# Optimization experiments

Hardware: AMD Instinct MI355X
Metric: run time of the kernel (lower is better)

## Reference

```python
import jax, jax.numpy as jnp
import numpy as np

B = 2048        # batch
D_DENSE = 13    # dense input features
F = 7           # number of sparse features
CARD = 10000    # cardinality per sparse feature (== len(tokenizer_values))
E = 64          # embedding dim per feature
D_OUT = 32      # dense arch output size
S_OUT = 32      # sparse arch output size per feature
D_HID = 2 * D_OUT   # DenseArch MLP hidden (output_size*2 per code)
S_HID = 2 * S_OUT   # SparseArch MLP hidden (output_size*2 per code)
CONCAT = D_OUT + F * S_OUT    # 256
P_IN = CONCAT * CONCAT        # 65536, flattened outer product
P_HID = 512


def setup_inputs() -> dict:
    key = jax.random.key(0)
    ks = jax.random.split(key, 18)
    s = 0.05
    return {
        "dense_features": jax.random.normal(ks[0], (B, D_DENSE), dtype=jnp.float32),
        "sparse_features": jax.random.randint(ks[1], (B, F), 0, CARD, dtype=jnp.int64),
        # tokenizer_values per feature (shared arange, as in metadata)
        "tokenizers": jnp.arange(CARD, dtype=jnp.int64),
        # embedding tables stacked over features: [F, CARD, E]
        "emb_tables": jax.random.normal(ks[2], (F, CARD, E), dtype=jnp.float32) * s,
        # DenseArch MLP
        "dw1": jax.random.normal(ks[3], (D_DENSE, D_HID), dtype=jnp.float32) * s,
        "db1": jnp.zeros((D_HID,), dtype=jnp.float32),
        "dw2": jax.random.normal(ks[4], (D_HID, D_OUT), dtype=jnp.float32) * s,
        "db2": jnp.zeros((D_OUT,), dtype=jnp.float32),
        # per-feature sparse MLPs stacked over features
        "sw1": jax.random.normal(ks[5], (F, E, S_HID), dtype=jnp.float32) * s,
        "sb1": jnp.zeros((F, S_HID), dtype=jnp.float32),
        "sw2": jax.random.normal(ks[6], (F, S_HID, S_OUT), dtype=jnp.float32) * s,
        "sb2": jnp.zeros((F, S_OUT), dtype=jnp.float32),
        # PredictionLayer MLP
        "pw1": jax.random.normal(ks[7], (P_IN, P_HID), dtype=jnp.float32) * s,
        "pb1": jnp.zeros((P_HID,), dtype=jnp.float32),
        "pw2": jax.random.normal(ks[8], (P_HID, 1), dtype=jnp.float32) * s,
        "pb2": jnp.zeros((1,), dtype=jnp.float32),
    }


def reference(dense_features, sparse_features, tokenizers, emb_tables,
              dw1, db1, dw2, db2, sw1, sb1, sw2, sb2, pw1, pb1, pw2, pb2):
    # DenseArch: MLP(13 -> 64 -> 32)
    dense_out = jnp.maximum(dense_features @ dw1 + db1, 0.0) @ dw2 + db2  # [B, D_OUT]

    # SparseArch: equality-match argmax indexing (faithful to get_indices),
    # then embedding gather and per-feature MLP, vectorized over features.
    matches = sparse_features[:, :, None] == tokenizers[None, None, :]  # [B, F, CARD]
    idx = jnp.argmax(matches, axis=2)                                   # [B, F]
    gathered = emb_tables[jnp.arange(emb_tables.shape[0])[None, :], idx]  # [B, F, E]
    h = jnp.maximum(jnp.einsum('bfe,feh->bfh', gathered, sw1) + sb1, 0.0)
    sparse_out = jnp.einsum('bfh,fho->bfo', h, sw2) + sb2                # [B, F, S_OUT]

    # DenseSparseInteractionLayer: concat -> outer product -> flatten
    concat = jnp.concatenate(
        [dense_out, sparse_out.reshape(sparse_out.shape[0], -1)], axis=1)  # [B, CONCAT]
    outer = jnp.einsum('bi,bj->bij', concat, concat)
    flattened = outer.reshape(concat.shape[0], -1)                       # [B, CONCAT^2]

    # PredictionLayer: MLP(CONCAT^2 -> P_HID -> 1) + sigmoid, squeeze
    logits = jnp.maximum(flattened @ pw1 + pb1, 0.0) @ pw2 + pb2
    return jax.nn.sigmoid(logits).squeeze()
```

## Files before the change

kernel.cpp:

```cpp
#include <hip/hip_runtime.h>
#include <hip/hip_fp16.h>
#include <math.h>

#define BATCH 2048
#define NFEAT 7
#define CARD 10000
#define CONCAT 256
#define P_HID 512

#define BM 128
#define BN 128
#define BK 64
#define KSPLIT 10
#define NUNITS 640
#define UNIT_ST (512 * 64)
#define PREP_BLOCKS (NUNITS * 2)

using f16x4   = __attribute__((ext_vector_type(4))) _Float16;
using half8   = __attribute__((ext_vector_type(8))) _Float16;
using floatx4 = __attribute__((ext_vector_type(4))) float;

__device__ __forceinline__ void dma16(const _Float16* g, _Float16* l) {
    __builtin_amdgcn_global_load_lds(
        (const __attribute__((address_space(1))) unsigned int*)g,
        (__attribute__((address_space(3))) unsigned int*)l,
        16, 0, 0);
}

__device__ __forceinline__ void unit_decode(int u, int& i, int& jw) {
    if (u < 64)       { i = u;                          jw = 0; }
    else if (u < 192) { i = (u < 128) ? u : u - 128;    jw = 1; }
    else if (u < 384) { i = (u < 256) ? u - 64 : u - 256; jw = 2; }
    else              { i = (u < 448) ? u - 192 : u - 448; jw = 3; }
}

__global__ __launch_bounds__(256) void fused_pre(
    const float* __restrict__ dense, const int* __restrict__ sparse,
    const float* __restrict__ emb,
    const float* __restrict__ dw1, const float* __restrict__ db1,
    const float* __restrict__ dw2, const float* __restrict__ db2,
    const float* __restrict__ sw1, const float* __restrict__ sb1,
    const float* __restrict__ sw2, const float* __restrict__ sb2,
    const float* __restrict__ pw1,
    _Float16* __restrict__ cbf, _Float16* __restrict__ St)
{
    __shared__ __align__(16) _Float16 sh[64 * 256];
    const int tid = threadIdx.x;

    if (blockIdx.x < PREP_BLOCKS) {
        const int u = blockIdx.x >> 1, nh = blockIdx.x & 1;
        const int nb = nh * 256;
        int i, jw;
        unit_decode(u, i, jw);

#pragma unroll
        for (int m = 0; m < 16; ++m) {
            const int flat = m * 256 + tid;
            const int q = flat >> 6, c4 = flat & 63;
            const int j = (jw << 6) + q;
            floatx4 s = {0.f, 0.f, 0.f, 0.f};
            if (j >= i) {
                s = __builtin_nontemporal_load(
                    (const floatx4*)(pw1 + ((size_t)i * 256 + j) * P_HID + nb + 4 * c4));
                if (j > i) {
                    const floatx4 mv = __builtin_nontemporal_load(
                        (const floatx4*)(pw1 + ((size_t)j * 256 + i) * P_HID + nb + 4 * c4));
                    s += mv;
                }
            }
            f16x4 hv = {(_Float16)s.x, (_Float16)s.y, (_Float16)s.z, (_Float16)s.w};
            *(f16x4*)(sh + q * 256 + 4 * c4) = hv;
        }
        __syncthreads();

        const _Float16* col = sh + tid;
        _Float16* outp = St + (size_t)u * UNIT_ST + (size_t)(nb + tid) * 64;
#pragma unroll
        for (int e = 0; e < 8; ++e) {
            half8 o;
#pragma unroll
            for (int r = 0; r < 8; ++r) o[r] = col[(8 * e + r) * 256];
            *(half8*)(outp + 8 * e) = o;
        }
    } else {
        float* smem = (float*)sh;
        const int wv = tid >> 6, t = tid & 63;
        const int b = (blockIdx.x - PREP_BLOCKS) * 4 + wv;
        float* xs   = smem + wv * 13;
        float* bufA = smem + 64  + wv * 64;
        float* bufB = smem + 320 + wv * 64;

        if (t < 13) xs[t] = dense[b * 13 + t];
        __syncthreads();

        float h = db1[t];
#pragma unroll
        for (int d = 0; d < 13; ++d) h += xs[d] * dw1[d * 64 + t];
        bufA[t] = fmaxf(h, 0.f);
        __syncthreads();

        if (t < 32) {
            float o = db2[t];
#pragma unroll
            for (int k = 0; k < 64; ++k) o += bufA[k] * dw2[k * 32 + t];
            cbf[b * 256 + t] = (_Float16)o;
        }

        for (int f = 0; f < NFEAT; ++f) {
            __syncthreads();
            const int idx = sparse[b * NFEAT + f];
            bufB[t] = emb[((size_t)(f * CARD + idx)) * 64 + t];
            __syncthreads();
            float s = sb1[f * 64 + t];
#pragma unroll
            for (int e = 0; e < 64; ++e) s += bufB[e] * sw1[(f * 64 + e) * 64 + t];
            bufA[t] = fmaxf(s, 0.f);
            __syncthreads();
            if (t < 32) {
                float o = sb2[f * 32 + t];
#pragma unroll
                for (int k = 0; k < 64; ++k) o += bufA[k] * sw2[(f * 64 + k) * 32 + t];
                cbf[b * 256 + 32 + f * 32 + t] = (_Float16)o;
            }
        }
    }
}

__global__ __launch_bounds__(256, 3) void bilinear_gemm(
    const _Float16* __restrict__ cbf, const _Float16* __restrict__ St,
    _Float16* __restrict__ hidpart)
{
    __shared__ _Float16 Bl[3][BN][BK];

    const int b = blockIdx.x;
    const int xcd = b & 7, slot = b >> 3;
    const int mt = slot & 15;
    const int slice = ((slot >> 4) << 3) | xcd;
    const int nt = slice & 3, ks = slice >> 2;
    const int m0 = mt * BM, n0 = nt * BN;
    const int t0 = ks * 64;
    const int jws = (int)((0x3333222110ULL >> (ks * 4)) & 0xF);

    const int tid = threadIdx.x, lane = tid & 63, wv = tid >> 6;
    const int wrow = (wv & 1) * 64, wcol = (wv >> 1) * 64;
    const int l15 = lane & 15, l4 = lane >> 4, l7 = lane & 7;

    floatx4 acc[4][4];
#pragma unroll
    for (int i = 0; i < 4; ++i)
#pragma unroll
        for (int j = 0; j < 4; ++j) acc[i][j] = (floatx4){0.f, 0.f, 0.f, 0.f};

    const _Float16* arow0 = cbf + (size_t)(m0 + wrow + l15) * 256;

    half8 pre[4][2];
#pragma unroll
    for (int i = 0; i < 4; ++i)
#pragma unroll
        for (int kh = 0; kh < 2; ++kh)
            pre[i][kh] = *(const half8*)(arow0 + i * 4096 + (jws << 6)
                                         + kh * 32 + l4 * 8);

    const int drow = wv * 32 + (lane >> 3);
    const int eswz = (lane & 7) ^ ((lane >> 3) & 7);
    const _Float16* bsrc = St + (size_t)t0 * UNIT_ST + (size_t)(n0 + drow) * 64 + eswz * 8;

    _Float16 ciA[4], ciB[4];

    {
        int iu0, jj0; unit_decode(t0, iu0, jj0);
#pragma unroll
        for (int i = 0; i < 4; ++i) ciA[i] = arow0[i * 4096 + iu0];
    }
#pragma unroll
    for (int p = 0; p < 4; ++p)
        dma16(bsrc + (size_t)(p * 8) * 64, &Bl[0][wv * 32 + p * 8][0]);
#pragma unroll
    for (int p = 0; p < 4; ++p)
        dma16(bsrc + UNIT_ST + (size_t)(p * 8) * 64, &Bl[1][wv * 32 + p * 8][0]);
    bsrc += (size_t)2 * UNIT_ST;
    asm volatile("s_waitcnt vmcnt(4)" ::: "memory");
    __builtin_amdgcn_s_barrier();

#define GBODY(IT, CIC, CIN, CUR)                                               \
    {                                                                          \
        const int it_ = (IT);                                                  \
        const int bnx2_ = (CUR) ? (CUR) - 1 : 2;                \
        if (it_ + 1 < 64) {                                                    \
            int iu_, jj_; unit_decode(t0 + it_ + 1, iu_, jj_);                 \
            _Pragma("unroll")                                                  \
            for (int i = 0; i < 4; ++i) CIN[i] = arow0[i * 4096 + iu_];        \
        }                                                                      \
        if (it_ + 2 < 64) {                                                    \
            _Pragma("unroll")                                                  \
            for (int p = 0; p < 4; ++p)                                        \
                dma16(bsrc + (size_t)(p * 8) * 64,                             \
                      &Bl[bnx2_][wv * 32 + p * 8][0]);                         \
            bsrc += UNIT_ST;                                                   \
        }                                                                      \
        __builtin_amdgcn_s_setprio(1);                                         \
        _Pragma("unroll")                                                      \
        for (int kh = 0; kh < 2; ++kh) {                                       \
            half8 af[4], bfr[4];                                               \
            _Pragma("unroll")                                                  \
            for (int i = 0; i < 4; ++i) {                                      \
                const _Float16 c_ = CIC[i];                                    \
                const half8 cv_ = {c_, c_, c_, c_, c_, c_, c_, c_};            \
                af[i] = pre[i][kh] * cv_;                                      \
            }                                                                  \
            const int s_ = ((kh * 4 + l4) ^ l7) * 8;                           \
            _Pragma("unroll")                                                  \
            for (int j = 0; j < 4; ++j)                                        \
                bfr[j] = *(const half8*)&Bl[CUR][wcol + j * 16 + l15][s_];     \
            _Pragma("unroll")                                                  \
            for (int i = 0; i < 4; ++i)                                        \
                _Pragma("unroll")                                              \
                for (int j = 0; j < 4; ++j)                                    \
                    acc[i][j] = __builtin_amdgcn_mfma_f32_16x16x32_f16(        \
                        af[i], bfr[j], acc[i][j], 0, 0, 0);                    \
        }                                                                      \
        __builtin_amdgcn_s_setprio(0);                                         \
        if (it_ + 2 < 64)                                                      \
            asm volatile("s_waitcnt vmcnt(8)" ::: "memory");                   \
        else if (it_ + 1 < 64)                                                 \
            asm volatile("s_waitcnt vmcnt(4)" ::: "memory");                   \
        else                                                                   \
            asm volatile("s_waitcnt vmcnt(0)" ::: "memory");                   \
        __builtin_amdgcn_s_barrier();                                          \
        __builtin_amdgcn_sched_barrier(0);                                     \
    }

    int bc = 0;
    for (int it2 = 0; it2 < 64; it2 += 2) {
        GBODY(it2, ciA, ciB, bc);
        const int bc1 = (bc < 2) ? bc + 1 : 0;
        GBODY(it2 + 1, ciB, ciA, bc1);
        bc = (bc1 < 2) ? bc1 + 1 : 0;
    }
#undef GBODY

    _Float16* outp = hidpart + (size_t)ks * BATCH * P_HID;
    const int r0 = m0 + wrow + l4 * 4;
    const int c0 = n0 + wcol + l15;
#pragma unroll
    for (int i = 0; i < 4; ++i)
#pragma unroll
        for (int j = 0; j < 4; ++j)
#pragma unroll
            for (int r = 0; r < 4; ++r)
                outp[(size_t)(r0 + i * 16 + r) * P_HID + c0 + j * 16] =
                    (_Float16)acc[i][j][r];
}

__global__ __launch_bounds__(256) void finalize(
    const _Float16* __restrict__ hidpart,
    const float* __restrict__ pb1,
    const float* __restrict__ pw2,
    const float* __restrict__ pb2,
    float* __restrict__ out)
{
    const int b = blockIdx.x, t = threadIdx.x;
    const int wv = t >> 6, lane = t & 63;

    float acc[8];
#pragma unroll
    for (int k = 0; k < 8; ++k) acc[k] = 0.f;

    for (int s = wv; s < KSPLIT; s += 4) {
        const half8 v = *(const half8*)(hidpart + (size_t)s * BATCH * P_HID
                                        + (size_t)b * P_HID + lane * 8);
#pragma unroll
        for (int k = 0; k < 8; ++k) acc[k] += (float)v[k];
    }

    __shared__ float red[4 * 512];
#pragma unroll
    for (int k = 0; k < 8; ++k) red[wv * 512 + k * 64 + lane] = acc[k];
    __syncthreads();

    if (wv == 0) {
        float dot = 0.f;
#pragma unroll
        for (int k = 0; k < 8; ++k) {
            const int n = lane * 8 + k;
            float v = red[k * 64 + lane] + red[512 + k * 64 + lane]
                    + red[1024 + k * 64 + lane] + red[1536 + k * 64 + lane];
            v += pb1[n];
            v = fmaxf(v, 0.f);
            dot += v * pw2[n];
        }
#pragma unroll
        for (int off = 32; off; off >>= 1) dot += __shfl_down(dot, off, 64);
        if (lane == 0) {
            const float s = dot + pb2[0];
            out[b] = 1.f / (1.f + expf(-s));
        }
    }
}

extern "C" void kernel_launch(void* const* d_in, const int* in_sizes, int n_in,
                              void* d_out, int out_size, void* d_ws, size_t ws_size,
                              hipStream_t stream)
{
    const float* dense  = (const float*)d_in[0];
    const int*   sparse = (const int*)d_in[1];
    const float* emb = (const float*)d_in[3];
    const float* dw1 = (const float*)d_in[4];
    const float* db1 = (const float*)d_in[5];
    const float* dw2 = (const float*)d_in[6];
    const float* db2 = (const float*)d_in[7];
    const float* sw1 = (const float*)d_in[8];
    const float* sb1 = (const float*)d_in[9];
    const float* sw2 = (const float*)d_in[10];
    const float* sb2 = (const float*)d_in[11];
    const float* pw1 = (const float*)d_in[12];
    const float* pb1 = (const float*)d_in[13];
    const float* pw2 = (const float*)d_in[14];
    const float* pb2 = (const float*)d_in[15];

    char* ws = (char*)d_ws;
    _Float16* cbf     = (_Float16*)ws;
    _Float16* St      = (_Float16*)(ws + (1 << 20));
    _Float16* hidpart = (_Float16*)(ws + (1 << 20) + ((size_t)40 << 20));

    fused_pre<<<PREP_BLOCKS + BATCH / 4, 256, 0, stream>>>(
        dense, sparse, emb, dw1, db1, dw2, db2, sw1, sb1, sw2, sb2, pw1,
        cbf, St);
    bilinear_gemm<<<16 * 4 * KSPLIT, 256, 0, stream>>>(cbf, St, hidpart);
    finalize<<<BATCH, 256, 0, stream>>>(hidpart, pb1, pw2, pb2, (float*)d_out);
}
```

Before: 378.9 us.

## Enlarge bilinear GEMM tiles to 256x256 and stage scaled A in shared memory

The bilinear GEMM moves from 128x128 tiles with 4 waves to 256x256 tiles with 8 waves and 16 K-splits of 40 units each, using a new unit ordering. The scaled A operand (concat row times a per-unit scalar) is now built cooperatively into a double-buffered, swizzled LDS tile instead of being recomputed per wave in registers. B prefetch drops from triple to double buffering. The aim is more data reuse per tile and fewer redundant A multiplies, at the cost of more registers per thread, more LDS, fewer blocks in flight, and more partial sums for finalize to reduce.

```diff
diff --git a/kernel.cpp b/kernel.cpp
--- a/kernel.cpp
+++ b/kernel.cpp
@@ -8,10 +8,11 @@
 #define CONCAT 256
 #define P_HID 512
 
-#define BM 128
-#define BN 128
+#define BM 256
+#define BN 256
 #define BK 64
-#define KSPLIT 10
+#define KSPLIT 16
+#define NTILES 40
 #define NUNITS 640
 #define UNIT_ST (512 * 64)
 #define PREP_BLOCKS (NUNITS * 2)
@@ -28,10 +29,10 @@
 }
 
 __device__ __forceinline__ void unit_decode(int u, int& i, int& jw) {
-    if (u < 64)       { i = u;                          jw = 0; }
-    else if (u < 192) { i = (u < 128) ? u : u - 128;    jw = 1; }
-    else if (u < 384) { i = (u < 256) ? u - 64 : u - 256; jw = 2; }
-    else              { i = (u < 448) ? u - 192 : u - 448; jw = 3; }
+    if (u < 256)      { i = u;                jw = u >> 6; }
+    else if (u < 448) { int v = u - 256; i = v / 3;        jw = 1 + v % 3; }
+    else if (u < 576) { int v = u - 448; i = 64 + (v >> 1); jw = 2 + (v & 1); }
+    else              { i = 128 + (u - 576); jw = 3; }
 }
 
 __global__ __launch_bounds__(256) void fused_pre(
@@ -126,124 +127,142 @@
     }
 }
 
-__global__ __launch_bounds__(256, 3) void bilinear_gemm(
+__global__ __launch_bounds__(512, 2) void bilinear_gemm(
     const _Float16* __restrict__ cbf, const _Float16* __restrict__ St,
     _Float16* __restrict__ hidpart)
 {
-    __shared__ _Float16 Bl[3][BN][BK];
+    __shared__ __align__(16) _Float16 Albuf[2][BM * BK];
+    __shared__ _Float16 Bl[2][BN][BK];
 
     const int b = blockIdx.x;
     const int xcd = b & 7, slot = b >> 3;
-    const int mt = slot & 15;
-    const int slice = ((slot >> 4) << 3) | xcd;
-    const int nt = slice & 3, ks = slice >> 2;
+    const int mt = slot & 7;
+    const int slice = ((slot >> 3) << 3) | xcd;
+    const int nt = slice & 1, ks = slice >> 1;
     const int m0 = mt * BM, n0 = nt * BN;
-    const int t0 = ks * 64;
-    const int jws = (int)((0x3333222110ULL >> (ks * 4)) & 0xF);
+    const int t0 = ks * NTILES;
 
     const int tid = threadIdx.x, lane = tid & 63, wv = tid >> 6;
-    const int wrow = (wv & 1) * 64, wcol = (wv >> 1) * 64;
+    const int wrow = (wv & 1) * 128, wcol = (wv >> 1) * 64;
     const int l15 = lane & 15, l4 = lane >> 4, l7 = lane & 7;
-
-    floatx4 acc[4][4];
-#pragma unroll
-    for (int i = 0; i < 4; ++i)
+    const int arow = tid >> 1, ajoff = (tid & 1) * 32;
+
+    floatx4 acc[8][4];
+#pragma unroll
+    for (int i = 0; i < 8; ++i)
 #pragma unroll
         for (int j = 0; j < 4; ++j) acc[i][j] = (floatx4){0.f, 0.f, 0.f, 0.f};
 
-    const _Float16* arow0 = cbf + (size_t)(m0 + wrow + l15) * 256;
-
-    half8 pre[4][2];
-#pragma unroll
-    for (int i = 0; i < 4; ++i)
-#pragma unroll
-        for (int kh = 0; kh < 2; ++kh)
-            pre[i][kh] = *(const half8*)(arow0 + i * 4096 + (jws << 6)
-                                         + kh * 32 + l4 * 8);
+    const _Float16* crow = cbf + (m0 + arow) * 256;
+
+    half8 pre[4][4];
+#pragma unroll
+    for (int jw = 0; jw < 4; ++jw)
+#pragma unroll
+        for (int x = 0; x < 4; ++x)
+            pre[jw][x] = *(const half8*)(crow + (jw << 6) + ajoff + 8 * x);
+
+    const int awsz = (arow & 7) << 4;
 
     const int drow = wv * 32 + (lane >> 3);
     const int eswz = (lane & 7) ^ ((lane >> 3) & 7);
     const _Float16* bsrc = St + (size_t)t0 * UNIT_ST + (size_t)(n0 + drow) * 64 + eswz * 8;
 
-    _Float16 ciA[4], ciB[4];
+#define AGEN(NB, JW, C)                                                        \
+    {                                                                          \
+        const half8 civ_ = {C, C, C, C, C, C, C, C};                           \
+        char* aw_ = (char*)Albuf[NB] + arow * 128;                             \
+        *(half8*)(aw_ + ((ajoff * 2 +  0) ^ awsz)) = pre[JW][0] * civ_;        \
+        *(half8*)(aw_ + ((ajoff * 2 + 16) ^ awsz)) = pre[JW][1] * civ_;        \
+        *(half8*)(aw_ + ((ajoff * 2 + 32) ^ awsz)) = pre[JW][2] * civ_;        \
+        *(half8*)(aw_ + ((ajoff * 2 + 48) ^ awsz)) = pre[JW][3] * civ_;        \
+    }
+#define AGEN_SW(NB, JW, C)                                                     \
+    switch (JW) {                                                              \
+        case 0:  AGEN(NB, 0, C); break;                                        \
+        case 1:  AGEN(NB, 1, C); break;                                        \
+        case 2:  AGEN(NB, 2, C); break;                                        \
+        default: AGEN(NB, 3, C); break;                                        \
+    }
+
+    _Float16 ciA, ciB;
 
     {
-        int iu0, jj0; unit_decode(t0, iu0, jj0);
-#pragma unroll
-        for (int i = 0; i < 4; ++i) ciA[i] = arow0[i * 4096 + iu0];
-    }
-#pragma unroll
-    for (int p = 0; p < 4; ++p)
-        dma16(bsrc + (size_t)(p * 8) * 64, &Bl[0][wv * 32 + p * 8][0]);
-#pragma unroll
-    for (int p = 0; p < 4; ++p)
-        dma16(bsrc + UNIT_ST + (size_t)(p * 8) * 64, &Bl[1][wv * 32 + p * 8][0]);
-    bsrc += (size_t)2 * UNIT_ST;
-    asm volatile("s_waitcnt vmcnt(4)" ::: "memory");
+        int ui0, ujw0; unit_decode(t0, ui0, ujw0);
+        const _Float16 ci0 = crow[ui0];
+#pragma unroll
+        for (int p = 0; p < 4; ++p)
+            dma16(bsrc + (size_t)(p * 8) * 64, &Bl[0][wv * 32 + p * 8][0]);
+        bsrc += UNIT_ST;
+        AGEN_SW(0, ujw0, ci0);
+        int ui1, ujw1; unit_decode(t0 + 1, ui1, ujw1);
+        ciA = crow[ui1];
+    }
+    asm volatile("s_waitcnt vmcnt(1) lgkmcnt(0)" ::: "memory");
     __builtin_amdgcn_s_barrier();
+    __builtin_amdgcn_sched_barrier(0);
 
 #define GBODY(IT, CIC, CIN, CUR)                                               \
     {                                                                          \
         const int it_ = (IT);                                                  \
-        const int bnx2_ = (CUR) ? (CUR) - 1 : 2;                \
-        if (it_ + 1 < 64) {                                                    \
-            int iu_, jj_; unit_decode(t0 + it_ + 1, iu_, jj_);                 \
-            _Pragma("unroll")                                                  \
-            for (int i = 0; i < 4; ++i) CIN[i] = arow0[i * 4096 + iu_];        \
-        }                                                                      \
-        if (it_ + 2 < 64) {                                                    \
+        if (it_ + 1 < NTILES) {                                                \
             _Pragma("unroll")                                                  \
             for (int p = 0; p < 4; ++p)                                        \
                 dma16(bsrc + (size_t)(p * 8) * 64,                             \
-                      &Bl[bnx2_][wv * 32 + p * 8][0]);                         \
+                      &Bl[(CUR) ^ 1][wv * 32 + p * 8][0]);                     \
             bsrc += UNIT_ST;                                                   \
+            int ujw1_, ui1_; unit_decode(t0 + it_ + 1, ui1_, ujw1_);           \
+            AGEN_SW((CUR) ^ 1, ujw1_, CIC);                                    \
+        }                                                                      \
+        if (it_ + 2 < NTILES) {                                                \
+            int ui2_, ujw2_; unit_decode(t0 + it_ + 2, ui2_, ujw2_);           \
+            CIN = crow[ui2_];                                                  \
         }                                                                      \
         __builtin_amdgcn_s_setprio(1);                                         \
         _Pragma("unroll")                                                      \
         for (int kh = 0; kh < 2; ++kh) {                                       \
-            half8 af[4], bfr[4];                                               \
+            half8 af[8], bfr[4];                                               \
             _Pragma("unroll")                                                  \
-            for (int i = 0; i < 4; ++i) {                                      \
-                const _Float16 c_ = CIC[i];                                    \
-                const half8 cv_ = {c_, c_, c_, c_, c_, c_, c_, c_};            \
-                af[i] = pre[i][kh] * cv_;                                      \
+            for (int i = 0; i < 8; ++i) {                                      \
+                const int r_ = wrow + i * 16 + l15;                            \
+                const int cb_ = (kh * 64 + l4 * 16) ^ ((r_ & 7) << 4);         \
+                af[i] = *(const half8*)((const char*)Albuf[CUR] + r_ * 128 + cb_); \
             }                                                                  \
             const int s_ = ((kh * 4 + l4) ^ l7) * 8;                           \
             _Pragma("unroll")                                                  \
             for (int j = 0; j < 4; ++j)                                        \
                 bfr[j] = *(const half8*)&Bl[CUR][wcol + j * 16 + l15][s_];     \
             _Pragma("unroll")                                                  \
-            for (int i = 0; i < 4; ++i)                                        \
+            for (int i = 0; i < 8; ++i)                                        \
                 _Pragma("unroll")                                              \
                 for (int j = 0; j < 4; ++j)                                    \
                     acc[i][j] = __builtin_amdgcn_mfma_f32_16x16x32_f16(        \
                         af[i], bfr[j], acc[i][j], 0, 0, 0);                    \
         }                                                                      \
         __builtin_amdgcn_s_setprio(0);                                         \
-        if (it_ + 2 < 64)                                                      \
-            asm volatile("s_waitcnt vmcnt(8)" ::: "memory");                   \
-        else if (it_ + 1 < 64)                                                 \
-            asm volatile("s_waitcnt vmcnt(4)" ::: "memory");                   \
-        else                                                                   \
-            asm volatile("s_waitcnt vmcnt(0)" ::: "memory");                   \
-        __builtin_amdgcn_s_barrier();                                          \
-        __builtin_amdgcn_sched_barrier(0);                                     \
-    }
-
-    int bc = 0;
-    for (int it2 = 0; it2 < 64; it2 += 2) {
-        GBODY(it2, ciA, ciB, bc);
-        const int bc1 = (bc < 2) ? bc + 1 : 0;
-        GBODY(it2 + 1, ciB, ciA, bc1);
-        bc = (bc1 < 2) ? bc1 + 1 : 0;
+        if (it_ + 1 < NTILES) {                                                \
+            if (it_ + 2 < NTILES)                                              \
+                asm volatile("s_waitcnt vmcnt(1) lgkmcnt(0)" ::: "memory");    \
+            else                                                               \
+                asm volatile("s_waitcnt vmcnt(0) lgkmcnt(0)" ::: "memory");    \
+            __builtin_amdgcn_s_barrier();                                      \
+            __builtin_amdgcn_sched_barrier(0);                                 \
+        }                                                                      \
+    }
+
+    for (int it2 = 0; it2 < NTILES; it2 += 2) {
+        GBODY(it2,     ciA, ciB, 0);
+        GBODY(it2 + 1, ciB, ciA, 1);
     }
 #undef GBODY
+#undef AGEN_SW
+#undef AGEN
 
     _Float16* outp = hidpart + (size_t)ks * BATCH * P_HID;
     const int r0 = m0 + wrow + l4 * 4;
     const int c0 = n0 + wcol + l15;
 #pragma unroll
-    for (int i = 0; i < 4; ++i)
+    for (int i = 0; i < 8; ++i)
 #pragma unroll
         for (int j = 0; j < 4; ++j)
 #pragma unroll
@@ -266,7 +285,9 @@
 #pragma unroll
     for (int k = 0; k < 8; ++k) acc[k] = 0.f;
 
-    for (int s = wv; s < KSPLIT; s += 4) {
+#pragma unroll
+    for (int si = 0; si < 4; ++si) {
+        const int s = wv + 4 * si;
         const half8 v = *(const half8*)(hidpart + (size_t)s * BATCH * P_HID
                                         + (size_t)b * P_HID + lane * 8);
 #pragma unroll
@@ -326,6 +347,6 @@
     fused_pre<<<PREP_BLOCKS + BATCH / 4, 256, 0, stream>>>(
         dense, sparse, emb, dw1, db1, dw2, db2, sw1, sb1, sw2, sb2, pw1,
         cbf, St);
-    bilinear_gemm<<<16 * 4 * KSPLIT, 256, 0, stream>>>(cbf, St, hidpart);
+    bilinear_gemm<<<8 * 2 * KSPLIT, 512, 0, stream>>>(cbf, St, hidpart);
     finalize<<<BATCH, 256, 0, stream>>>(hidpart, pb1, pw2, pb2, (float*)d_out);
 }
```

New measurement: 378.0 us. No clear change (-0.2%).
